# Kernel tuning notes

Measured on AMD Instinct MI355X. Metric: run time of the kernel, lower is better.

The kernel has to match this reference:

```python
import jax, jax.numpy as jnp
import numpy as np

HIDDEN = 1024
NUM_HEADS = 8
HEAD_DIM = HIDDEN // NUM_HEADS
MAX_BACKWARD = 11   # context_left - 1
MAX_FORWARD = 12    # context_right
SPAN = MAX_BACKWARD + MAX_FORWARD + 1  # 24

B, U, W, C = 8, 16, 128, 151


def setup_inputs() -> dict:
    key = jax.random.key(0)
    kq, kk, kp = jax.random.split(key, 3)
    queries = jax.random.normal(kq, (B, U, W, NUM_HEADS, HEAD_DIM), dtype=jnp.float32)
    keys = jax.random.normal(kk, (B, U, C, NUM_HEADS, HEAD_DIM), dtype=jnp.float32)
    # glorot-ish scale for pos_proj (hidden, num_heads*head_dim)
    pos_proj = jax.random.normal(kp, (HIDDEN, NUM_HEADS * HEAD_DIM), dtype=jnp.float32) * (1.0 / np.sqrt(HIDDEN))
    return {"queries": queries, "keys": keys, "pos_proj": pos_proj}


def _sinusoid_emb(pos_proj):
    # positions: max_backward .. -max_forward (descending), shape (SPAN,)
    pos = jnp.arange(MAX_BACKWARD, -(MAX_FORWARD + 1), -1, dtype=jnp.float32)
    num_ts = HIDDEN // 2
    inv_ts = jnp.ones((num_ts,), dtype=jnp.float32)  # module uses ones
    scaled = pos[:, None] * inv_ts[None, :]          # (SPAN, HIDDEN/2)
    signal = jnp.concatenate([jnp.sin(scaled), jnp.cos(scaled)], axis=-1)  # (SPAN, HIDDEN)
    proj = signal @ pos_proj                         # (SPAN, N*H)
    return proj.reshape(SPAN, NUM_HEADS, HEAD_DIM)


def _relative_shift(term_bd, context_size):
    # term_bd: (B, N, U, W, SPAN) -> (B, N, U, W, C)
    b, n, u, w, _ = term_bd.shape
    pad = context_size + 1 - SPAN
    padded = jnp.pad(term_bd, ((0, 0), (0, 0), (0, 0), (0, 0), (0, pad)))
    flat = padded.reshape(b, n, u, w * (context_size + 1))
    sliced = flat[:, :, :, : w * context_size]
    return sliced.reshape(b, n, u, w, context_size)


def reference(queries, keys, pos_proj):
    context_size = keys.shape[2]
    sin_emb = _sinusoid_emb(pos_proj)                      # (SPAN, N, H)
    qp = jnp.transpose(queries, (0, 3, 1, 2, 4))           # (B, N, U, W, H)
    kp = jnp.transpose(keys, (0, 3, 1, 4, 2))              # (B, N, U, H, C)
    term_ac = jnp.matmul(qp, kp)                           # (B, N, U, W, C)
    # term_bd: query-position interaction, (B, N, U, W, SPAN)
    term_bd = jnp.einsum("bnuwh,fnh->bnuwf", qp, sin_emb)
    term_bd = _relative_shift(term_bd, context_size)       # (B, N, U, W, C)
    return term_ac + term_bd
```

## Files before the change

### kernel.cpp

```cpp
#include <hip/hip_runtime.h>
#include <cmath>

#define NHEADS 8
#define HDIM 128
#define SPAN 24
#define U_ 16
#define W_ 128
#define C_ 151
#define HID 1024

typedef unsigned short ushort8v __attribute__((ext_vector_type(8)));
typedef __bf16 bf16x8 __attribute__((ext_vector_type(8)));
typedef float f32x4 __attribute__((ext_vector_type(4)));

__device__ inline unsigned short f2bf(float f) {
    union { float f; unsigned u; } v; v.f = f;
    unsigned r = v.u + 0x7FFFu + ((v.u >> 16) & 1u);
    return (unsigned short)(r >> 16);
}
__device__ inline float bf2f(unsigned short u) {
    union { unsigned u; float f; } v; v.u = ((unsigned)u) << 16;
    return v.f;
}
__device__ inline ushort8v cvt8(float4 a, float4 b) {
    ushort8v v;
    v[0] = f2bf(a.x); v[1] = f2bf(a.y); v[2] = f2bf(a.z); v[3] = f2bf(a.w);
    v[4] = f2bf(b.x); v[5] = f2bf(b.y); v[6] = f2bf(b.z); v[7] = f2bf(b.w);
    return v;
}

__global__ void k_partial(const float* __restrict__ pp, float* __restrict__ part) {
    const int t = threadIdx.x;
    const int row0 = blockIdx.x * 16;
    float4 s = make_float4(0.f, 0.f, 0.f, 0.f);
    #pragma unroll
    for (int i = 0; i < 16; ++i) {
        float4 v = *(const float4*)(pp + (size_t)(row0 + i) * HID + t * 4);
        s.x += v.x; s.y += v.y; s.z += v.z; s.w += v.w;
    }
    *(float4*)(part + (size_t)blockIdx.x * HID + t * 4) = s;
}

struct SC { float s[SPAN]; float c[SPAN]; };

__global__ void k_emb(const float* __restrict__ part, float* __restrict__ emb, SC sc) {
    const int j = blockIdx.x * 256 + threadIdx.x;
    float s1 = 0.f, s2 = 0.f;
    #pragma unroll 4
    for (int i = 0; i < 32; ++i) s1 += part[(size_t)i * HID + j];
    #pragma unroll 4
    for (int i = 32; i < 64; ++i) s2 += part[(size_t)i * HID + j];
    #pragma unroll
    for (int f = 0; f < SPAN; ++f)
        emb[(size_t)f * HID + j] = sc.s[f] * s1 + sc.c[f] * s2;
}

#define KEXT_BYTES (176 * 256)
#define BD_PITCH 25

__global__ __launch_bounds__(512, 4) void k_main(const float* __restrict__ q,
                                                 const float* __restrict__ k,
                                                 const float* __restrict__ embf,
                                                 float* __restrict__ out) {
    __shared__ __align__(16) char lds_raw[KEXT_BYTES + W_ * BD_PITCH * 2];
    unsigned short* bd = (unsigned short*)(lds_raw + KEXT_BYTES);

    const int bid = blockIdx.x;
    const int n = bid & 7;
    const int u = (bid >> 3) & 15;
    const int b = bid >> 7;

    const size_t qbase = ((size_t)(b * U_ + u) * W_) * HID + n * HDIM;
    const size_t kbase = ((size_t)(b * U_ + u) * C_) * HID + n * HDIM;
    const size_t obase = ((size_t)((b * NHEADS + n) * U_ + u)) * (W_ * C_);

    const int tid = threadIdx.x;
    const int lane = tid & 63;
    const int wave = tid >> 6;
    const int w0 = wave * 16;
    const int lr = lane & 15;
    const int lk = lane >> 4;

    float4 pf0[5], pf1[5], pt0, pt1;
    #pragma unroll
    for (int it = 0; it < 5; ++it) {
        const int ui = it * 512 + tid;
        const int r = ui >> 4, u16 = ui & 15;
        const float* src = (r < C_)
            ? (k + kbase + (size_t)r * HID + u16 * 8)
            : (embf + (size_t)(r - C_) * HID + n * HDIM + u16 * 8);
        pf0[it] = *(const float4*)src;
        pf1[it] = *(const float4*)(src + 4);
    }
    if (tid < 256) {
        const int r = 160 + (tid >> 4), u16 = tid & 15;
        if (r < 175) {
            const float* src = embf + (size_t)(r - C_) * HID + n * HDIM + u16 * 8;
            pt0 = *(const float4*)src;
            pt1 = *(const float4*)(src + 4);
        }
    }
    const float* qrow = q + qbase + (size_t)(w0 + lr) * HID + lk * 8;
    float4 qpf[8];
    #pragma unroll
    for (int kk = 0; kk < 4; ++kk) {
        qpf[2 * kk]     = *(const float4*)(qrow + kk * 32);
        qpf[2 * kk + 1] = *(const float4*)(qrow + kk * 32 + 4);
    }

    #pragma unroll
    for (int it = 0; it < 5; ++it) {
        const int ui = it * 512 + tid;
        const int r = ui >> 4, u16 = ui & 15;
        const int dst = r * 256 + ((u16 * 16) ^ ((r & 7) << 4));
        *(ushort8v*)(lds_raw + dst) = cvt8(pf0[it], pf1[it]);
    }
    if (tid < 256) {
        const int r = 160 + (tid >> 4), u16 = tid & 15;
        const int dst = r * 256 + ((u16 * 16) ^ ((r & 7) << 4));
        ushort8v v_;
        if (r < 175) v_ = cvt8(pt0, pt1);
        else         v_ = (ushort8v)(unsigned short)0;
        *(ushort8v*)(lds_raw + dst) = v_;
    }

    bf16x8 qf[4];
    #pragma unroll
    for (int kk = 0; kk < 4; ++kk)
        qf[kk] = __builtin_bit_cast(bf16x8, cvt8(qpf[2 * kk], qpf[2 * kk + 1]));

    __syncthreads();

    f32x4 acc[11];
    #pragma unroll
    for (int j = 0; j < 11; ++j) acc[j] = (f32x4)(0.f);

    #pragma unroll
    for (int kk = 0; kk < 4; ++kk) {
        #pragma unroll
        for (int j = 0; j < 11; ++j) {
            const int r = j * 16 + lr;
            const int byt = r * 256 + (((kk * 64) + (lk * 16)) ^ ((r & 7) << 4));
            bf16x8 bf = __builtin_bit_cast(bf16x8, *(const ushort8v*)(lds_raw + byt));
            acc[j] = __builtin_amdgcn_mfma_f32_16x16x32_bf16(qf[kk], bf, acc[j], 0, 0, 0);
        }
    }

    {
        const int c9 = 144 + lr;
        if (c9 >= C_) {
            const int f = c9 - C_;
            #pragma unroll
            for (int reg = 0; reg < 4; ++reg) {
                const int w = w0 + lk * 4 + reg;
                bd[w * BD_PITCH + f] = f2bf(acc[9][reg]);
            }
        }
        const int f10 = 9 + lr;
        if (f10 < SPAN) {
            #pragma unroll
            for (int reg = 0; reg < 4; ++reg) {
                const int w = w0 + lk * 4 + reg;
                bd[w * BD_PITCH + f10] = f2bf(acc[10][reg]);
            }
        }
    }

    #pragma unroll
    for (int j = 0; j < 10; ++j) {
        const int c = j * 16 + lr;
        if (c < C_) {
            #pragma unroll
            for (int reg = 0; reg < 4; ++reg) {
                const int w = w0 + lk * 4 + reg;
                float v = acc[j][reg];
                const int d = c - w;
                if (d >= 0 && d < SPAN) v += bf2f(bd[w * BD_PITCH + d]);
                out[obase + (size_t)w * C_ + c] = v;
            }
        }
    }
}

extern "C" void kernel_launch(void* const* d_in, const int* in_sizes, int n_in,
                              void* d_out, int out_size, void* d_ws, size_t ws_size,
                              hipStream_t stream) {
    const float* queries = (const float*)d_in[0];
    const float* keys    = (const float*)d_in[1];
    const float* posproj = (const float*)d_in[2];
    float* out = (float*)d_out;

    float* part = (float*)d_ws;
    float* embf = (float*)((char*)d_ws + 64 * HID * 4);

    SC sc;
    for (int f = 0; f < SPAN; ++f) {
        float p = (float)(11 - f);
        sc.s[f] = sinf(p);
        sc.c[f] = cosf(p);
    }

    k_partial<<<64, 256, 0, stream>>>(posproj, part);
    k_emb<<<4, 256, 0, stream>>>(part, embf, sc);
    k_main<<<1024, 512, 0, stream>>>(queries, keys, embf, out);
}
```

Before: 57.45 us.

## Fuse sinusoid embedding reduction into main kernel, dropping separate k_emb launch

Removes the k_emb kernel and has every k_main block rebuild its head's 24 embedding rows in LDS. Each block reads the 64 partial row-sums for its head slice and reduces them in two LDS stages, then combines them with the sin/cos coefficients. This saves one kernel launch and its serial dependency, but adds redundant per-block global reads of partials, two extra __syncthreads, and bf16 rounding of intermediate sums, which reduces precision.

Measured after the change: 50.90 us. 1.13x faster.

```diff
diff --git a/kernel.cpp b/kernel.cpp
--- a/kernel.cpp
+++ b/kernel.cpp
@@ -10,6 +10,7 @@
 #define HID 1024
 
 typedef unsigned short ushort8v __attribute__((ext_vector_type(8)));
+typedef unsigned short ushort4v __attribute__((ext_vector_type(4)));
 typedef __bf16 bf16x8 __attribute__((ext_vector_type(8)));
 typedef float f32x4 __attribute__((ext_vector_type(4)));
 
@@ -43,25 +44,15 @@
 
 struct SC { float s[SPAN]; float c[SPAN]; };
 
-__global__ void k_emb(const float* __restrict__ part, float* __restrict__ emb, SC sc) {
-    const int j = blockIdx.x * 256 + threadIdx.x;
-    float s1 = 0.f, s2 = 0.f;
-    #pragma unroll 4
-    for (int i = 0; i < 32; ++i) s1 += part[(size_t)i * HID + j];
-    #pragma unroll 4
-    for (int i = 32; i < 64; ++i) s2 += part[(size_t)i * HID + j];
-    #pragma unroll
-    for (int f = 0; f < SPAN; ++f)
-        emb[(size_t)f * HID + j] = sc.s[f] * s1 + sc.c[f] * s2;
-}
-
 #define KEXT_BYTES (176 * 256)
 #define BD_PITCH 25
+#define AUX_OFF KEXT_BYTES
+#define S12_OFF (KEXT_BYTES + 4096)
 
 __global__ __launch_bounds__(512, 4) void k_main(const float* __restrict__ q,
                                                  const float* __restrict__ k,
-                                                 const float* __restrict__ embf,
-                                                 float* __restrict__ out) {
+                                                 const float* __restrict__ part,
+                                                 float* __restrict__ out, SC sc) {
     __shared__ __align__(16) char lds_raw[KEXT_BYTES + W_ * BD_PITCH * 2];
     unsigned short* bd = (unsigned short*)(lds_raw + KEXT_BYTES);
 
@@ -81,25 +72,22 @@
     const int lr = lane & 15;
     const int lk = lane >> 4;
 
-    float4 pf0[5], pf1[5], pt0, pt1;
+    float4 pf0[5], pf1[5];
     #pragma unroll
     for (int it = 0; it < 5; ++it) {
         const int ui = it * 512 + tid;
         const int r = ui >> 4, u16 = ui & 15;
-        const float* src = (r < C_)
-            ? (k + kbase + (size_t)r * HID + u16 * 8)
-            : (embf + (size_t)(r - C_) * HID + n * HDIM + u16 * 8);
-        pf0[it] = *(const float4*)src;
-        pf1[it] = *(const float4*)(src + 4);
-    }
-    if (tid < 256) {
-        const int r = 160 + (tid >> 4), u16 = tid & 15;
-        if (r < 175) {
-            const float* src = embf + (size_t)(r - C_) * HID + n * HDIM + u16 * 8;
-            pt0 = *(const float4*)src;
-            pt1 = *(const float4*)(src + 4);
-        }
-    }
+        if (r < C_) {
+            const float* src = k + kbase + (size_t)r * HID + u16 * 8;
+            pf0[it] = *(const float4*)src;
+            pf1[it] = *(const float4*)(src + 4);
+        }
+    }
+    const int c4 = tid & 31, rg = tid >> 5;
+    float4 pp4[4];
+    #pragma unroll
+    for (int i = 0; i < 4; ++i)
+        pp4[i] = *(const float4*)(part + (size_t)(rg * 4 + i) * HID + n * HDIM + c4 * 4);
     const float* qrow = q + qbase + (size_t)(w0 + lr) * HID + lk * 8;
     float4 qpf[8];
     #pragma unroll
@@ -112,18 +100,52 @@
     for (int it = 0; it < 5; ++it) {
         const int ui = it * 512 + tid;
         const int r = ui >> 4, u16 = ui & 15;
+        if (r < C_) {
+            const int dst = r * 256 + ((u16 * 16) ^ ((r & 7) << 4));
+            *(ushort8v*)(lds_raw + dst) = cvt8(pf0[it], pf1[it]);
+        }
+    }
+    {
+        float4 rs;
+        rs.x = pp4[0].x + pp4[1].x + pp4[2].x + pp4[3].x;
+        rs.y = pp4[0].y + pp4[1].y + pp4[2].y + pp4[3].y;
+        rs.z = pp4[0].z + pp4[1].z + pp4[2].z + pp4[3].z;
+        rs.w = pp4[0].w + pp4[1].w + pp4[2].w + pp4[3].w;
+        ushort4v rb;
+        rb[0] = f2bf(rs.x); rb[1] = f2bf(rs.y); rb[2] = f2bf(rs.z); rb[3] = f2bf(rs.w);
+        *(ushort4v*)(lds_raw + AUX_OFF + rg * 256 + c4 * 8) = rb;
+    }
+    __syncthreads();
+
+    if (tid < 256) {
+        const int col = tid & 127, half = tid >> 7;
+        float s = 0.f;
+        #pragma unroll
+        for (int g = 0; g < 8; ++g)
+            s += bf2f(*(const unsigned short*)(lds_raw + AUX_OFF + (half * 8 + g) * 256 + col * 2));
+        *(float*)(lds_raw + S12_OFF + (half * 128 + col) * 4) = s;
+    }
+    __syncthreads();
+
+    if (tid < 384) {
+        const int f = tid >> 4, u16 = tid & 15;
+        const int r = C_ + f;
+        const float sf = sc.s[f], cf = sc.c[f];
+        ushort8v v;
+        #pragma unroll
+        for (int e = 0; e < 8; ++e) {
+            const int col = u16 * 8 + e;
+            const float S1 = *(const float*)(lds_raw + S12_OFF + col * 4);
+            const float S2 = *(const float*)(lds_raw + S12_OFF + 512 + col * 4);
+            v[e] = f2bf(sf * S1 + cf * S2);
+        }
         const int dst = r * 256 + ((u16 * 16) ^ ((r & 7) << 4));
-        *(ushort8v*)(lds_raw + dst) = cvt8(pf0[it], pf1[it]);
-    }
-    if (tid < 256) {
-        const int r = 160 + (tid >> 4), u16 = tid & 15;
+        *(ushort8v*)(lds_raw + dst) = v;
+    } else if (tid < 400) {
+        const int u16 = tid - 384, r = 175;
         const int dst = r * 256 + ((u16 * 16) ^ ((r & 7) << 4));
-        ushort8v v_;
-        if (r < 175) v_ = cvt8(pt0, pt1);
-        else         v_ = (ushort8v)(unsigned short)0;
-        *(ushort8v*)(lds_raw + dst) = v_;
-    }
-
+        *(ushort8v*)(lds_raw + dst) = (ushort8v)(unsigned short)0;
+    }
     bf16x8 qf[4];
     #pragma unroll
     for (int kk = 0; kk < 4; ++kk)
@@ -191,7 +213,6 @@
     float* out = (float*)d_out;
 
     float* part = (float*)d_ws;
-    float* embf = (float*)((char*)d_ws + 64 * HID * 4);
 
     SC sc;
     for (int f = 0; f < SPAN; ++f) {
@@ -201,6 +222,5 @@
     }
 
     k_partial<<<64, 256, 0, stream>>>(posproj, part);
-    k_emb<<<4, 256, 0, stream>>>(part, embf, sc);
-    k_main<<<1024, 512, 0, stream>>>(queries, keys, embf, out);
-}
+    k_main<<<1024, 512, 0, stream>>>(queries, keys, part, out, sc);
+}
```
